# Optimization experiments

Measured on AMD Instinct MI355X. Metric: run time of the kernel, lower is better.

## Reference

```python
import jax, jax.numpy as jnp
import numpy as np

H = 8        # heads
DH = 64      # dim_head
EPS = 1e-5   # LayerNorm eps (torch default)


def setup_inputs() -> dict:
    key = jax.random.key(0)
    k0, k1, k2, k3, k4 = jax.random.split(key, 5)
    b, l, n, dim = 2, 8, 256, 512
    inner = H * DH
    return {
        "xyzs": jax.random.normal(k0, (b, l, n, 3), dtype=jnp.float32),
        "features": jax.random.normal(k1, (b, l, n, dim), dtype=jnp.float32),
        "ln_gamma": jnp.ones((dim,), dtype=jnp.float32),
        "ln_beta": jnp.zeros((dim,), dtype=jnp.float32),
        "w_qkv": jax.random.normal(k2, (dim, 3 * inner), dtype=jnp.float32) * 0.02,
        "w_sp": jax.random.normal(k3, (3, DH), dtype=jnp.float32) * 0.3,
        "w_out": jax.random.normal(k4, (inner, dim), dtype=jnp.float32) * 0.02,
        "b_out": jnp.zeros((dim,), dtype=jnp.float32),
    }


def reference(xyzs, features, ln_gamma, ln_beta, w_qkv, w_sp, w_out, b_out):
    b, l, n, dim = features.shape
    m = l * n
    inner = H * DH
    scale = DH ** (-0.5)

    # LayerNorm over last dim (biased variance, eps=1e-5)
    mu = jnp.mean(features, axis=-1, keepdims=True)
    var = jnp.var(features, axis=-1, keepdims=True)
    normed = (features - mu) * jax.lax.rsqrt(var + EPS) * ln_gamma + ln_beta

    # qkv projection, chunk into q,k,v, reshape 'b l n (h d) -> b h (l n) d'
    qkv = normed.reshape(b, m, dim) @ w_qkv            # [b, m, 3*inner]
    def split_heads(t):
        return t.reshape(b, m, H, DH).transpose(0, 2, 1, 3)  # [b, h, m, d]
    q = split_heads(qkv[..., :inner])
    k = split_heads(qkv[..., inner:2 * inner])
    v = split_heads(qkv[..., 2 * inner:])

    dots = jnp.einsum('bhid,bhjd->bhij', q, k) * scale  # [b, h, m, m]
    attn = jax.nn.softmax(dots, axis=-1)
    v_out = jnp.einsum('bhij,bhjd->bhid', attn, v)      # [b, h, m, d]

    # pairwise coordinate deltas: delta[b,i,j,c] = xyz[b,j,c] - xyz[b,i,c]
    xyz_f = xyzs.reshape(b, m, 3)
    delta = xyz_f[:, None, :, :] - xyz_f[:, :, None, :]  # [b, m, m, 3]
    # attention-weighted aggregation over j (avoids [b,h,m,m,3] intermediate)
    agg = jnp.einsum('bhij,bijc->bhic', attn, delta)     # [b, h, m, 3]
    disp = agg @ w_sp                                    # [b, h, m, DH]

    out = v_out + disp                                   # [b, h, m, DH]
    out = out.transpose(0, 2, 1, 3).reshape(b, m, inner) # 'b h m d -> b m (h d)'
    out = jax.nn.gelu(out @ w_out + b_out, approximate=False)
    return out.reshape(b, l, n, dim) + features
```

## Files before the change

### kernel.cpp

```cpp
#include <hip/hip_runtime.h>
#include <hip/hip_bf16.h>
#include <math.h>

#define BB   2
#define MM   2048
#define DIM  512
#define NH   8
#define DHd  64
#define NQK  1536
#define ROWS 4096
#define NROW 32768
#define SPLITK 3

typedef __hip_bfloat16 bf16;
typedef __attribute__((ext_vector_type(8))) short bf16x8;
typedef __attribute__((ext_vector_type(4))) float f32x4;
typedef __attribute__((ext_vector_type(16))) float f32x16;
typedef __attribute__((ext_vector_type(8))) unsigned short us8;
typedef __attribute__((ext_vector_type(4))) unsigned int u32x4;

__device__ __forceinline__ unsigned short f2bf_bits(float x) {
    bf16 h = __float2bfloat16(x);
    return *(unsigned short*)&h;
}
__device__ __forceinline__ float bf2f(unsigned short u) {
    unsigned int v = ((unsigned int)u) << 16;
    return __uint_as_float(v);
}
__device__ __forceinline__ unsigned cvtpk_bf16(float lo, float hi) {
    unsigned r;
    asm("v_cvt_pk_bf16_f32 %0, %1, %2" : "=v"(r) : "v"(lo), "v"(hi));
    return r;
}
__device__ __forceinline__ void pl32swap(unsigned &a, unsigned &b) {
    asm volatile("v_permlane32_swap_b32 %0, %1" : "+v"(a), "+v"(b));
}

__global__ __launch_bounds__(256) void pre_kernel(
    const float* __restrict__ feat, const float* __restrict__ gamma,
    const float* __restrict__ beta, unsigned short* __restrict__ normed,
    const float* __restrict__ wqkv, const float* __restrict__ wout,
    unsigned short* __restrict__ wqkvT, unsigned short* __restrict__ woutT)
{
    __shared__ float st[64][65];
    int b = blockIdx.x;
    int tid = threadIdx.x;
    if (b < ROWS / 4) {
        int w = tid >> 6, lane = tid & 63;
        int row = b * 4 + w;
        const float* fr = feat + (size_t)row * DIM + lane * 8;
        float4 v0 = *(const float4*)fr;
        float4 v1 = *(const float4*)(fr + 4);
        float s  = v0.x + v0.y + v0.z + v0.w + v1.x + v1.y + v1.z + v1.w;
        float ss = v0.x*v0.x + v0.y*v0.y + v0.z*v0.z + v0.w*v0.w
                 + v1.x*v1.x + v1.y*v1.y + v1.z*v1.z + v1.w*v1.w;
        #pragma unroll
        for (int o = 32; o >= 1; o >>= 1) { s += __shfl_xor(s, o); ss += __shfl_xor(ss, o); }
        float mu  = s * (1.0f / DIM);
        float var = ss * (1.0f / DIM) - mu * mu;
        float inv = rsqrtf(var + 1e-5f);
        const float* gp = gamma + lane * 8;
        const float* bp = beta  + lane * 8;
        float4 g0 = *(const float4*)gp, g1 = *(const float4*)(gp + 4);
        float4 e0 = *(const float4*)bp, e1 = *(const float4*)(bp + 4);
        unsigned short ov[8];
        ov[0] = f2bf_bits((v0.x - mu) * inv * g0.x + e0.x);
        ov[1] = f2bf_bits((v0.y - mu) * inv * g0.y + e0.y);
        ov[2] = f2bf_bits((v0.z - mu) * inv * g0.z + e0.z);
        ov[3] = f2bf_bits((v0.w - mu) * inv * g0.w + e0.w);
        ov[4] = f2bf_bits((v1.x - mu) * inv * g1.x + e1.x);
        ov[5] = f2bf_bits((v1.y - mu) * inv * g1.y + e1.y);
        ov[6] = f2bf_bits((v1.z - mu) * inv * g1.z + e1.z);
        ov[7] = f2bf_bits((v1.w - mu) * inv * g1.w + e1.w);
        *(us8*)&normed[(size_t)row * DIM + lane * 8] = *(us8*)ov;
        return;
    }
    int idx = b - ROWS / 4;
    const float* in; unsigned short* out; int N, n0;
    if (idx < 192) { in = wqkv; out = wqkvT; N = NQK; n0 = (idx >> 3) * 64; }
    else { idx -= 192; in = wout; out = woutT; N = DIM; n0 = (idx >> 3) * 64; }
    int k0 = (idx & 7) * 64;
    #pragma unroll
    for (int p = 0; p < 16; p++) {
        int e = tid + p * 256;
        int r = e >> 6, c = e & 63;
        st[r][c] = in[(size_t)(k0 + r) * N + n0 + c];
    }
    __syncthreads();
    #pragma unroll
    for (int p = 0; p < 16; p++) {
        int e = tid + p * 256;
        int nr = e >> 6, kc = e & 63;
        out[(size_t)(n0 + nr) * DIM + k0 + kc] = f2bf_bits(st[kc][nr]);
    }
}

__global__ __launch_bounds__(256) void qkv_gemm(
    const unsigned short* __restrict__ A, const unsigned short* __restrict__ BT,
    unsigned short* __restrict__ qd, unsigned short* __restrict__ kd,
    unsigned short* __restrict__ vd)
{
    __shared__ __align__(16) unsigned short sA[128 * 72];
    __shared__ __align__(16) unsigned short sB[64 * 72];
    int tid = threadIdx.x;
    int r0 = blockIdx.x * 128;
    int n0 = blockIdx.y * 64;
    int chunk = n0 >> 9;
    int h     = (n0 & 511) >> 6;
    int w = tid >> 6, lane = tid & 63;
    int wm = w >> 1, wn = w & 1;
    int ln15 = lane & 15, quad = lane >> 4;

    int arow = tid >> 1, acol = (tid & 1) * 32;
    int brow = tid >> 2, bcol = (tid & 3) * 16;

    f32x4 acc[4][2] = {};
    us8 ra[4], rb[2];

    #pragma unroll
    for (int u = 0; u < 4; u++)
        ra[u] = *(const us8*)&A[(size_t)(r0 + arow) * DIM + acol + u * 8];
    #pragma unroll
    for (int u = 0; u < 2; u++)
        rb[u] = *(const us8*)&BT[(size_t)(n0 + brow) * DIM + bcol + u * 8];

    for (int k0 = 0; k0 < DIM; k0 += 64) {
        __syncthreads();
        #pragma unroll
        for (int u = 0; u < 4; u++) *(us8*)&sA[arow * 72 + acol + u * 8] = ra[u];
        #pragma unroll
        for (int u = 0; u < 2; u++) *(us8*)&sB[brow * 72 + bcol + u * 8] = rb[u];
        __syncthreads();
        int kn = k0 + 64;
        if (kn < DIM) {
            #pragma unroll
            for (int u = 0; u < 4; u++)
                ra[u] = *(const us8*)&A[(size_t)(r0 + arow) * DIM + kn + acol + u * 8];
            #pragma unroll
            for (int u = 0; u < 2; u++)
                rb[u] = *(const us8*)&BT[(size_t)(n0 + brow) * DIM + kn + bcol + u * 8];
        }
        bf16x8 fa[4][2], fb[2][2];
        #pragma unroll
        for (int i = 0; i < 4; i++)
            #pragma unroll
            for (int kk = 0; kk < 2; kk++)
                fa[i][kk] = *(const bf16x8*)&sA[(wm * 64 + i * 16 + ln15) * 72 + kk * 32 + quad * 8];
        #pragma unroll
        for (int j = 0; j < 2; j++)
            #pragma unroll
            for (int kk = 0; kk < 2; kk++)
                fb[j][kk] = *(const bf16x8*)&sB[(wn * 32 + j * 16 + ln15) * 72 + kk * 32 + quad * 8];
        if (chunk == 2) {
            #pragma unroll
            for (int kk = 0; kk < 2; kk++)
                #pragma unroll
                for (int i = 0; i < 4; i++)
                    #pragma unroll
                    for (int j = 0; j < 2; j++)
                        acc[i][j] = __builtin_amdgcn_mfma_f32_16x16x32_bf16(fa[i][kk], fb[j][kk], acc[i][j], 0, 0, 0);
        } else {
            #pragma unroll
            for (int kk = 0; kk < 2; kk++)
                #pragma unroll
                for (int i = 0; i < 4; i++)
                    #pragma unroll
                    for (int j = 0; j < 2; j++)
                        acc[i][j] = __builtin_amdgcn_mfma_f32_16x16x32_bf16(fb[j][kk], fa[i][kk], acc[i][j], 0, 0, 0);
        }
    }

    if (chunk == 2) {
        #pragma unroll
        for (int i = 0; i < 4; i++) {
            int gm = r0 + wm * 64 + i * 16 + quad * 4;
            int bb = gm >> 11, mm = gm & 2047;
            #pragma unroll
            for (int j = 0; j < 2; j++) {
                int d = wn * 32 + j * 16 + ln15;
                ushort4 pk;
                pk.x = f2bf_bits(acc[i][j][0]);
                pk.y = f2bf_bits(acc[i][j][1]);
                pk.z = f2bf_bits(acc[i][j][2]);
                pk.w = f2bf_bits(acc[i][j][3]);
                *(ushort4*)&vd[((size_t)(bb * NH + h) * DHd + d) * MM + mm] = pk;
            }
        }
    } else {
        unsigned short* dst = (chunk == 0) ? qd : kd;
        float sc = (chunk == 0) ? 0.125f : 1.0f;
        #pragma unroll
        for (int i = 0; i < 4; i++) {
            int gm = r0 + wm * 64 + i * 16 + ln15;
            int bb = gm >> 11, mm = gm & 2047;
            #pragma unroll
            for (int j = 0; j < 2; j++) {
                int d0 = wn * 32 + j * 16 + quad * 4;
                ushort4 pk;
                pk.x = f2bf_bits(acc[i][j][0] * sc);
                pk.y = f2bf_bits(acc[i][j][1] * sc);
                pk.z = f2bf_bits(acc[i][j][2] * sc);
                pk.w = f2bf_bits(acc[i][j][3] * sc);
                *(ushort4*)&dst[((size_t)(bb * NH + h) * MM + mm) * DHd + d0] = pk;
            }
        }
    }
}

__global__ __launch_bounds__(256, 3) void attn_kernel(
    const unsigned short* __restrict__ qg, const unsigned short* __restrict__ kg,
    const unsigned short* __restrict__ vg, const float* __restrict__ xyzs,
    unsigned short* __restrict__ obuf, float* __restrict__ lbuf)
{
    __shared__ __align__(16) unsigned short sK[64 * 72];
    __shared__ __align__(16) unsigned short sVT[96 * 72];

    int tid = threadIdx.x;
    int bh = blockIdx.y; int bb = bh >> 3;
    int i0 = blockIdx.x * 128;
    int ks = blockIdx.z;
    int w = tid >> 6;
    int lane = tid & 63;
    int ln31 = lane & 31;
    int hi   = lane >> 5;
    int hi8  = hi * 8;

    for (int e = tid; e < 28 * 72; e += 256) sVT[68 * 72 + e] = 0;
    if (tid < 64) sVT[67 * 72 + tid] = 0x3F80;

    bf16x8 aq[4];
    {
        const unsigned short* q0 = qg + ((size_t)bh * MM + i0 + w * 32 + ln31) * DHd + hi8;
        #pragma unroll
        for (int kc = 0; kc < 4; kc++)
            aq[kc] = *(const bf16x8*)(q0 + kc * 16);
    }

    f32x16 ot[3] = {};

    const unsigned short* kbase = kg + (size_t)bh * MM * DHd;
    const unsigned short* vbase = vg + (size_t)bh * DHd * MM;
    int jbeg = ks * 704;
    int jend = (ks == 2) ? MM : jbeg + 704;

    int srow = tid >> 2, scol16 = (tid & 3) * 16;

    us8 rk0, rk1, rv0, rv1;
    float rx = 0.f;
    {
        const unsigned short* src = kbase + (size_t)jbeg * DHd;
        rk0 = *(const us8*)&src[(size_t)tid * 16];
        rk1 = *(const us8*)&src[(size_t)tid * 16 + 8];
        const unsigned short* vs = vbase + jbeg;
        rv0 = *(const us8*)&vs[(size_t)srow * MM + scol16];
        rv1 = *(const us8*)&vs[(size_t)srow * MM + scol16 + 8];
        if (tid < 192) rx = xyzs[((size_t)bb * MM + jbeg) * 3 + tid];
    }

    for (int jt = jbeg; jt < jend; jt += 64) {
        __syncthreads();
        *(us8*)&sK[srow * 72 + scol16]      = rk0;
        *(us8*)&sK[srow * 72 + scol16 + 8]  = rk1;
        *(us8*)&sVT[srow * 72 + scol16]     = rv0;
        *(us8*)&sVT[srow * 72 + scol16 + 8] = rv1;
        if (tid < 192) {
            int key = tid / 3, c = tid - key * 3;
            sVT[(64 + c) * 72 + key] = f2bf_bits(rx);
        }
        __syncthreads();
        int jn = jt + 64;
        if (jn < jend) {
            const unsigned short* src = kbase + (size_t)jn * DHd;
            rk0 = *(const us8*)&src[(size_t)tid * 16];
            rk1 = *(const us8*)&src[(size_t)tid * 16 + 8];
            const unsigned short* vs = vbase + jn;
            rv0 = *(const us8*)&vs[(size_t)srow * MM + scol16];
            rv1 = *(const us8*)&vs[(size_t)srow * MM + scol16 + 8];
            if (tid < 192) rx = xyzs[((size_t)bb * MM + jn) * 3 + tid];
        }

        #pragma unroll
        for (int b = 0; b < 2; b++) {
            f32x16 zz = {};
            #pragma unroll
            for (int kc = 0; kc < 4; kc++) {
                bf16x8 kf = *(const bf16x8*)&sK[(b * 32 + ln31) * 72 + kc * 16 + hi8];
                zz = __builtin_amdgcn_mfma_f32_32x32x16_bf16(kf, aq[kc], zz, 0, 0, 0);
            }
            unsigned c_[8];
            #pragma unroll
            for (int j = 0; j < 8; j++)
                c_[j] = cvtpk_bf16(__expf(zz[2 * j]), __expf(zz[2 * j + 1]));
            unsigned x0 = c_[0], x2 = c_[2]; pl32swap(x0, x2);
            unsigned x1 = c_[1], x3 = c_[3]; pl32swap(x1, x3);
            unsigned y0 = c_[4], y2 = c_[6]; pl32swap(y0, y2);
            unsigned y1 = c_[5], y3 = c_[7]; pl32swap(y1, y3);
            u32x4 xv = {x0, x1, x2, x3};
            u32x4 yv = {y0, y1, y2, y3};
            bf16x8 X = *(bf16x8*)&xv;
            bf16x8 Y = *(bf16x8*)&yv;
            #pragma unroll
            for (int vb = 0; vb < 3; vb++) {
                bf16x8 v0 = *(const bf16x8*)&sVT[(vb * 32 + ln31) * 72 + b * 32 + hi8];
                bf16x8 v1 = *(const bf16x8*)&sVT[(vb * 32 + ln31) * 72 + b * 32 + 16 + hi8];
                ot[vb] = __builtin_amdgcn_mfma_f32_32x32x16_bf16(v0, X, ot[vb], 0, 0, 0);
                ot[vb] = __builtin_amdgcn_mfma_f32_32x32x16_bf16(v1, Y, ot[vb], 0, 0, 0);
            }
        }
    }

    size_t kso = (size_t)ks * NROW;
    size_t row = (size_t)bh * MM + i0 + w * 32 + ln31;
    unsigned short* orow = obuf + (kso + row) * 72;
    #pragma unroll
    for (int vb = 0; vb < 2; vb++) {
        #pragma unroll
        for (int rq = 0; rq < 4; rq++) {
            ushort4 pk;
            pk.x = f2bf_bits(ot[vb][rq * 4 + 0]);
            pk.y = f2bf_bits(ot[vb][rq * 4 + 1]);
            pk.z = f2bf_bits(ot[vb][rq * 4 + 2]);
            pk.w = f2bf_bits(ot[vb][rq * 4 + 3]);
            *(ushort4*)&orow[vb * 32 + rq * 8 + hi * 4] = pk;
        }
    }
    if (hi == 0) {
        orow[64] = f2bf_bits(ot[2][0]);
        orow[65] = f2bf_bits(ot[2][1]);
        orow[66] = f2bf_bits(ot[2][2]);
        lbuf[kso + row] = ot[2][3];
    }
}

__global__ __launch_bounds__(256) void merge_kernel(
    const unsigned short* __restrict__ obuf, const float* __restrict__ lbuf,
    const float* __restrict__ xyzs, const float* __restrict__ wsp,
    unsigned short* __restrict__ attn_out)
{
    __shared__ float sW[3][64];
    int tid = threadIdx.x;
    if (tid < 192) sW[tid >> 6][tid & 63] = wsp[tid];
    __syncthreads();
    int r   = blockIdx.x * 64 + (tid >> 2);
    int d0  = (tid & 3) * 16;
    int bh = r >> 11, qrow = r & 2047, bb = bh >> 3, hh = bh & 7;
    const unsigned short* p0 = obuf + (size_t)r * 72;
    const unsigned short* p1 = p0 + (size_t)NROW * 72;
    const unsigned short* p2 = p1 + (size_t)NROW * 72;
    float invl = 1.f / (lbuf[r] + lbuf[NROW + r] + lbuf[2 * NROW + r]);
    size_t xb = ((size_t)bb * MM + qrow) * 3;
    float gx = (bf2f(p0[64]) + bf2f(p1[64]) + bf2f(p2[64])) * invl - xyzs[xb + 0];
    float gy = (bf2f(p0[65]) + bf2f(p1[65]) + bf2f(p2[65])) * invl - xyzs[xb + 1];
    float gz = (bf2f(p0[66]) + bf2f(p1[66]) + bf2f(p2[66])) * invl - xyzs[xb + 2];
    us8 a0 = *(const us8*)&p0[d0];
    us8 a1 = *(const us8*)&p0[d0 + 8];
    us8 b0 = *(const us8*)&p1[d0];
    us8 b1 = *(const us8*)&p1[d0 + 8];
    us8 c0 = *(const us8*)&p2[d0];
    us8 c1 = *(const us8*)&p2[d0 + 8];
    unsigned short outv[16];
    #pragma unroll
    for (int e = 0; e < 8; e++) {
        int d = d0 + e;
        float v = (bf2f(a0[e]) + bf2f(b0[e]) + bf2f(c0[e])) * invl
                + gx * sW[0][d] + gy * sW[1][d] + gz * sW[2][d];
        outv[e] = f2bf_bits(v);
    }
    #pragma unroll
    for (int e = 0; e < 8; e++) {
        int d = d0 + 8 + e;
        float v = (bf2f(a1[e]) + bf2f(b1[e]) + bf2f(c1[e])) * invl
                + gx * sW[0][d] + gy * sW[1][d] + gz * sW[2][d];
        outv[8 + e] = f2bf_bits(v);
    }
    unsigned short* dst = attn_out + ((size_t)bb * MM + qrow) * DIM + hh * DHd + d0;
    *(us8*)dst       = *(us8*)&outv[0];
    *(us8*)(dst + 8) = *(us8*)&outv[8];
}

__global__ __launch_bounds__(256) void out_gemm(
    const unsigned short* __restrict__ A, const unsigned short* __restrict__ BT,
    const float* __restrict__ bias, const float* __restrict__ feat,
    float* __restrict__ out)
{
    __shared__ __align__(16) unsigned short sA[64 * 72];
    __shared__ __align__(16) unsigned short sB[64 * 72];
    int tid = threadIdx.x;
    int r0 = blockIdx.x * 64, n0 = blockIdx.y * 64;
    int w = tid >> 6, lane = tid & 63;
    int wm = w >> 1, wn = w & 1;
    int ln15 = lane & 15, quad = lane >> 4;

    int srow = tid >> 2, scol = (tid & 3) * 16;

    f32x4 acc[2][2] = {};
    us8 ra[2], rb[2];

    #pragma unroll
    for (int u = 0; u < 2; u++) {
        ra[u] = *(const us8*)&A[(size_t)(r0 + srow) * DIM + scol + u * 8];
        rb[u] = *(const us8*)&BT[(size_t)(n0 + srow) * DIM + scol + u * 8];
    }

    for (int k0 = 0; k0 < DIM; k0 += 64) {
        __syncthreads();
        #pragma unroll
        for (int u = 0; u < 2; u++) {
            *(us8*)&sA[srow * 72 + scol + u * 8] = ra[u];
            *(us8*)&sB[srow * 72 + scol + u * 8] = rb[u];
        }
        __syncthreads();
        int kn = k0 + 64;
        if (kn < DIM) {
            #pragma unroll
            for (int u = 0; u < 2; u++) {
                ra[u] = *(const us8*)&A[(size_t)(r0 + srow) * DIM + kn + scol + u * 8];
                rb[u] = *(const us8*)&BT[(size_t)(n0 + srow) * DIM + kn + scol + u * 8];
            }
        }
        bf16x8 af[2][2], bf_[2][2];
        #pragma unroll
        for (int i = 0; i < 2; i++)
            #pragma unroll
            for (int kk = 0; kk < 2; kk++)
                af[i][kk] = *(const bf16x8*)&sA[(wm * 32 + i * 16 + ln15) * 72 + kk * 32 + quad * 8];
        #pragma unroll
        for (int j = 0; j < 2; j++)
            #pragma unroll
            for (int kk = 0; kk < 2; kk++)
                bf_[j][kk] = *(const bf16x8*)&sB[(wn * 32 + j * 16 + ln15) * 72 + kk * 32 + quad * 8];
        #pragma unroll
        for (int kk = 0; kk < 2; kk++)
            #pragma unroll
            for (int i = 0; i < 2; i++)
                #pragma unroll
                for (int j = 0; j < 2; j++)
                    acc[i][j] = __builtin_amdgcn_mfma_f32_16x16x32_bf16(af[i][kk], bf_[j][kk], acc[i][j], 0, 0, 0);
    }

    #pragma unroll
    for (int i = 0; i < 2; i++) {
        #pragma unroll
        for (int reg = 0; reg < 4; reg++) {
            int gr = r0 + wm * 32 + i * 16 + quad * 4 + reg;
            #pragma unroll
            for (int j = 0; j < 2; j++) {
                int c = n0 + wn * 32 + j * 16 + ln15;
                float x = acc[i][j][reg] + bias[c];
                float g = 0.5f * x * (1.f + erff(x * 0.70710678118f));
                out[(size_t)gr * DIM + c] = g + feat[(size_t)gr * DIM + c];
            }
        }
    }
}

extern "C" void kernel_launch(void* const* d_in, const int* in_sizes, int n_in,
                              void* d_out, int out_size, void* d_ws, size_t ws_size,
                              hipStream_t stream)
{
    const float* xyzs  = (const float*)d_in[0];
    const float* feat  = (const float*)d_in[1];
    const float* gamma = (const float*)d_in[2];
    const float* beta  = (const float*)d_in[3];
    const float* wqkv  = (const float*)d_in[4];
    const float* wsp   = (const float*)d_in[5];
    const float* wout  = (const float*)d_in[6];
    const float* bout  = (const float*)d_in[7];
    float* out = (float*)d_out;

    unsigned short* ws16 = (unsigned short*)d_ws;
    const size_t SEGS = (size_t)ROWS * DIM;
    unsigned short* normed = ws16;
    unsigned short* qb     = ws16 + SEGS;
    unsigned short* kb     = ws16 + 2 * SEGS;
    unsigned short* vb     = ws16 + 3 * SEGS;
    unsigned short* wqkvT  = ws16 + 4 * SEGS;
    unsigned short* woutT  = wqkvT + (size_t)NQK * DIM;
    unsigned short* obuf   = woutT + (size_t)DIM * DIM;
    float*          lbuf   = (float*)(obuf + (size_t)SPLITK * NROW * 72);

    pre_kernel<<<ROWS / 4 + 256, 256, 0, stream>>>(feat, gamma, beta, normed,
                                                   wqkv, wout, wqkvT, woutT);
    qkv_gemm<<<dim3(32, 24), 256, 0, stream>>>(normed, wqkvT, qb, kb, vb);
    attn_kernel<<<dim3(16, 16, SPLITK), 256, 0, stream>>>(qb, kb, vb, xyzs, obuf, lbuf);
    merge_kernel<<<512, 256, 0, stream>>>(obuf, lbuf, xyzs, wsp, normed);
    out_gemm<<<dim3(64, 8), 256, 0, stream>>>(normed, woutT, bout, feat, out);
}
```

Measured before the change: 141.8 us.

## Drop split-K attention and fuse merge epilogue into attention kernel

```diff
diff --git a/kernel.cpp b/kernel.cpp
--- a/kernel.cpp
+++ b/kernel.cpp
@@ -9,8 +9,6 @@
 #define DHd  64
 #define NQK  1536
 #define ROWS 4096
-#define NROW 32768
-#define SPLITK 3
 
 typedef __hip_bfloat16 bf16;
 typedef __attribute__((ext_vector_type(8))) short bf16x8;
@@ -207,26 +205,27 @@
     }
 }
 
-__global__ __launch_bounds__(256, 3) void attn_kernel(
+__global__ __launch_bounds__(128, 1) void attn_kernel(
     const unsigned short* __restrict__ qg, const unsigned short* __restrict__ kg,
     const unsigned short* __restrict__ vg, const float* __restrict__ xyzs,
-    unsigned short* __restrict__ obuf, float* __restrict__ lbuf)
+    const float* __restrict__ wsp, unsigned short* __restrict__ attn_out)
 {
     __shared__ __align__(16) unsigned short sK[64 * 72];
     __shared__ __align__(16) unsigned short sVT[96 * 72];
+    __shared__ float sW[3][64];
 
     int tid = threadIdx.x;
-    int bh = blockIdx.y; int bb = bh >> 3;
-    int i0 = blockIdx.x * 128;
-    int ks = blockIdx.z;
+    int bh = blockIdx.y; int bb = bh >> 3; int hh = bh & 7;
+    int i0 = blockIdx.x * 64;
     int w = tid >> 6;
     int lane = tid & 63;
     int ln31 = lane & 31;
     int hi   = lane >> 5;
     int hi8  = hi * 8;
 
-    for (int e = tid; e < 28 * 72; e += 256) sVT[68 * 72 + e] = 0;
+    for (int e = tid; e < 28 * 72; e += 128) sVT[68 * 72 + e] = 0;
     if (tid < 64) sVT[67 * 72 + tid] = 0x3F80;
+    for (int e = tid; e < 192; e += 128) sW[e >> 6][e & 63] = wsp[e];
 
     bf16x8 aq[4];
     {
@@ -240,43 +239,47 @@
 
     const unsigned short* kbase = kg + (size_t)bh * MM * DHd;
     const unsigned short* vbase = vg + (size_t)bh * DHd * MM;
-    int jbeg = ks * 704;
-    int jend = (ks == 2) ? MM : jbeg + 704;
-
-    int srow = tid >> 2, scol16 = (tid & 3) * 16;
-
-    us8 rk0, rk1, rv0, rv1;
-    float rx = 0.f;
+
+    int srow = tid >> 1, scolB = (tid & 1) * 32;
+    int key0 = tid / 3, c0 = tid - key0 * 3;
+    int e1 = tid + 128;
+    int key1 = e1 / 3, c1 = e1 - key1 * 3;
+
+    us8 rk[4], rv[4];
+    float rx0 = 0.f, rx1 = 0.f;
     {
-        const unsigned short* src = kbase + (size_t)jbeg * DHd;
-        rk0 = *(const us8*)&src[(size_t)tid * 16];
-        rk1 = *(const us8*)&src[(size_t)tid * 16 + 8];
-        const unsigned short* vs = vbase + jbeg;
-        rv0 = *(const us8*)&vs[(size_t)srow * MM + scol16];
-        rv1 = *(const us8*)&vs[(size_t)srow * MM + scol16 + 8];
-        if (tid < 192) rx = xyzs[((size_t)bb * MM + jbeg) * 3 + tid];
-    }
-
-    for (int jt = jbeg; jt < jend; jt += 64) {
-        __syncthreads();
-        *(us8*)&sK[srow * 72 + scol16]      = rk0;
-        *(us8*)&sK[srow * 72 + scol16 + 8]  = rk1;
-        *(us8*)&sVT[srow * 72 + scol16]     = rv0;
-        *(us8*)&sVT[srow * 72 + scol16 + 8] = rv1;
-        if (tid < 192) {
-            int key = tid / 3, c = tid - key * 3;
-            sVT[(64 + c) * 72 + key] = f2bf_bits(rx);
-        }
+        const unsigned short* ks = kbase + (size_t)srow * DHd + scolB;
+        const unsigned short* vs = vbase + (size_t)srow * MM + scolB;
+        #pragma unroll
+        for (int u = 0; u < 4; u++) {
+            rk[u] = *(const us8*)(ks + u * 8);
+            rv[u] = *(const us8*)(vs + u * 8);
+        }
+        rx0 = xyzs[(size_t)bb * MM * 3 + tid];
+        if (tid < 64) rx1 = xyzs[(size_t)bb * MM * 3 + e1];
+    }
+
+    for (int jt = 0; jt < MM; jt += 64) {
+        __syncthreads();
+        #pragma unroll
+        for (int u = 0; u < 4; u++) {
+            *(us8*)&sK[srow * 72 + scolB + u * 8]  = rk[u];
+            *(us8*)&sVT[srow * 72 + scolB + u * 8] = rv[u];
+        }
+        sVT[(64 + c0) * 72 + key0] = f2bf_bits(rx0);
+        if (tid < 64) sVT[(64 + c1) * 72 + key1] = f2bf_bits(rx1);
         __syncthreads();
         int jn = jt + 64;
-        if (jn < jend) {
-            const unsigned short* src = kbase + (size_t)jn * DHd;
-            rk0 = *(const us8*)&src[(size_t)tid * 16];
-            rk1 = *(const us8*)&src[(size_t)tid * 16 + 8];
-            const unsigned short* vs = vbase + jn;
-            rv0 = *(const us8*)&vs[(size_t)srow * MM + scol16];
-            rv1 = *(const us8*)&vs[(size_t)srow * MM + scol16 + 8];
-            if (tid < 192) rx = xyzs[((size_t)bb * MM + jn) * 3 + tid];
+        if (jn < MM) {
+            const unsigned short* ks = kbase + (size_t)(jn + srow) * DHd + scolB;
+            const unsigned short* vs = vbase + (size_t)srow * MM + jn + scolB;
+            #pragma unroll
+            for (int u = 0; u < 4; u++) {
+                rk[u] = *(const us8*)(ks + u * 8);
+                rv[u] = *(const us8*)(vs + u * 8);
+            }
+            rx0 = xyzs[((size_t)bb * MM + jn) * 3 + tid];
+            if (tid < 64) rx1 = xyzs[((size_t)bb * MM + jn) * 3 + e1];
         }
 
         #pragma unroll
@@ -309,73 +312,29 @@
         }
     }
 
-    size_t kso = (size_t)ks * NROW;
-    size_t row = (size_t)bh * MM + i0 + w * 32 + ln31;
-    unsigned short* orow = obuf + (kso + row) * 72;
+    int gq = i0 + w * 32 + ln31;
+    float invl = 1.f / __shfl(ot[2][3], ln31);
+    size_t xb = ((size_t)bb * MM + gq) * 3;
+    float gx = __shfl(ot[2][0], ln31) * invl - xyzs[xb + 0];
+    float gy = __shfl(ot[2][1], ln31) * invl - xyzs[xb + 1];
+    float gz = __shfl(ot[2][2], ln31) * invl - xyzs[xb + 2];
+    unsigned short* dst = attn_out + ((size_t)bb * MM + gq) * DIM + hh * DHd;
     #pragma unroll
     for (int vb = 0; vb < 2; vb++) {
         #pragma unroll
         for (int rq = 0; rq < 4; rq++) {
+            int d0 = vb * 32 + rq * 8 + hi * 4;
             ushort4 pk;
-            pk.x = f2bf_bits(ot[vb][rq * 4 + 0]);
-            pk.y = f2bf_bits(ot[vb][rq * 4 + 1]);
-            pk.z = f2bf_bits(ot[vb][rq * 4 + 2]);
-            pk.w = f2bf_bits(ot[vb][rq * 4 + 3]);
-            *(ushort4*)&orow[vb * 32 + rq * 8 + hi * 4] = pk;
-        }
-    }
-    if (hi == 0) {
-        orow[64] = f2bf_bits(ot[2][0]);
-        orow[65] = f2bf_bits(ot[2][1]);
-        orow[66] = f2bf_bits(ot[2][2]);
-        lbuf[kso + row] = ot[2][3];
-    }
-}
-
-__global__ __launch_bounds__(256) void merge_kernel(
-    const unsigned short* __restrict__ obuf, const float* __restrict__ lbuf,
-    const float* __restrict__ xyzs, const float* __restrict__ wsp,
-    unsigned short* __restrict__ attn_out)
-{
-    __shared__ float sW[3][64];
-    int tid = threadIdx.x;
-    if (tid < 192) sW[tid >> 6][tid & 63] = wsp[tid];
-    __syncthreads();
-    int r   = blockIdx.x * 64 + (tid >> 2);
-    int d0  = (tid & 3) * 16;
-    int bh = r >> 11, qrow = r & 2047, bb = bh >> 3, hh = bh & 7;
-    const unsigned short* p0 = obuf + (size_t)r * 72;
-    const unsigned short* p1 = p0 + (size_t)NROW * 72;
-    const unsigned short* p2 = p1 + (size_t)NROW * 72;
-    float invl = 1.f / (lbuf[r] + lbuf[NROW + r] + lbuf[2 * NROW + r]);
-    size_t xb = ((size_t)bb * MM + qrow) * 3;
-    float gx = (bf2f(p0[64]) + bf2f(p1[64]) + bf2f(p2[64])) * invl - xyzs[xb + 0];
-    float gy = (bf2f(p0[65]) + bf2f(p1[65]) + bf2f(p2[65])) * invl - xyzs[xb + 1];
-    float gz = (bf2f(p0[66]) + bf2f(p1[66]) + bf2f(p2[66])) * invl - xyzs[xb + 2];
-    us8 a0 = *(const us8*)&p0[d0];
-    us8 a1 = *(const us8*)&p0[d0 + 8];
-    us8 b0 = *(const us8*)&p1[d0];
-    us8 b1 = *(const us8*)&p1[d0 + 8];
-    us8 c0 = *(const us8*)&p2[d0];
-    us8 c1 = *(const us8*)&p2[d0 + 8];
-    unsigned short outv[16];
-    #pragma unroll
-    for (int e = 0; e < 8; e++) {
-        int d = d0 + e;
-        float v = (bf2f(a0[e]) + bf2f(b0[e]) + bf2f(c0[e])) * invl
-                + gx * sW[0][d] + gy * sW[1][d] + gz * sW[2][d];
-        outv[e] = f2bf_bits(v);
-    }
-    #pragma unroll
-    for (int e = 0; e < 8; e++) {
-        int d = d0 + 8 + e;
-        float v = (bf2f(a1[e]) + bf2f(b1[e]) + bf2f(c1[e])) * invl
-                + gx * sW[0][d] + gy * sW[1][d] + gz * sW[2][d];
-        outv[8 + e] = f2bf_bits(v);
-    }
-    unsigned short* dst = attn_out + ((size_t)bb * MM + qrow) * DIM + hh * DHd + d0;
-    *(us8*)dst       = *(us8*)&outv[0];
-    *(us8*)(dst + 8) = *(us8*)&outv[8];
+            #pragma unroll
+            for (int j = 0; j < 4; j++) {
+                int d = d0 + j;
+                float v = ot[vb][rq * 4 + j] * invl
+                        + gx * sW[0][d] + gy * sW[1][d] + gz * sW[2][d];
+                ((unsigned short*)&pk)[j] = f2bf_bits(v);
+            }
+            *(ushort4*)&dst[d0] = pk;
+        }
+    }
 }
 
 __global__ __launch_bounds__(256) void out_gemm(
@@ -476,13 +435,10 @@
     unsigned short* vb     = ws16 + 3 * SEGS;
     unsigned short* wqkvT  = ws16 + 4 * SEGS;
     unsigned short* woutT  = wqkvT + (size_t)NQK * DIM;
-    unsigned short* obuf   = woutT + (size_t)DIM * DIM;
-    float*          lbuf   = (float*)(obuf + (size_t)SPLITK * NROW * 72);
 
     pre_kernel<<<ROWS / 4 + 256, 256, 0, stream>>>(feat, gamma, beta, normed,
                                                    wqkv, wout, wqkvT, woutT);
     qkv_gemm<<<dim3(32, 24), 256, 0, stream>>>(normed, wqkvT, qb, kb, vb);
-    attn_kernel<<<dim3(16, 16, SPLITK), 256, 0, stream>>>(qb, kb, vb, xyzs, obuf, lbuf);
-    merge_kernel<<<512, 256, 0, stream>>>(obuf, lbuf, xyzs, wsp, normed);
+    attn_kernel<<<dim3(32, 16), 128, 0, stream>>>(qb, kb, vb, xyzs, wsp, normed);
     out_gemm<<<dim3(64, 8), 256, 0, stream>>>(normed, woutT, bout, feat, out);
 }
```

Result: slower. 154.6 us (+9.0%).

## Split attention keys four ways, fold log2e into Q scale, use exp2

Applied to the files above, without the earlier changes.

```diff
diff --git a/kernel.cpp b/kernel.cpp
--- a/kernel.cpp
+++ b/kernel.cpp
@@ -10,7 +10,7 @@
 #define NQK  1536
 #define ROWS 4096
 #define NROW 32768
-#define SPLITK 3
+#define SPLITK 4
 
 typedef __hip_bfloat16 bf16;
 typedef __attribute__((ext_vector_type(8))) short bf16x8;
@@ -188,7 +188,7 @@
         }
     } else {
         unsigned short* dst = (chunk == 0) ? qd : kd;
-        float sc = (chunk == 0) ? 0.125f : 1.0f;
+        float sc = (chunk == 0) ? 0.18033688f : 1.0f;
         #pragma unroll
         for (int i = 0; i < 4; i++) {
             int gm = r0 + wm * 64 + i * 16 + ln15;
@@ -207,7 +207,7 @@
     }
 }
 
-__global__ __launch_bounds__(256, 3) void attn_kernel(
+__global__ __launch_bounds__(256, 4) void attn_kernel(
     const unsigned short* __restrict__ qg, const unsigned short* __restrict__ kg,
     const unsigned short* __restrict__ vg, const float* __restrict__ xyzs,
     unsigned short* __restrict__ obuf, float* __restrict__ lbuf)
@@ -219,7 +219,7 @@
     int bh = blockIdx.y; int bb = bh >> 3;
     int i0 = blockIdx.x * 128;
     int ks = blockIdx.z;
-    int w = tid >> 6;
+    int wid = tid >> 6;
     int lane = tid & 63;
     int ln31 = lane & 31;
     int hi   = lane >> 5;
@@ -230,7 +230,7 @@
 
     bf16x8 aq[4];
     {
-        const unsigned short* q0 = qg + ((size_t)bh * MM + i0 + w * 32 + ln31) * DHd + hi8;
+        const unsigned short* q0 = qg + ((size_t)bh * MM + i0 + wid * 32 + ln31) * DHd + hi8;
         #pragma unroll
         for (int kc = 0; kc < 4; kc++)
             aq[kc] = *(const bf16x8*)(q0 + kc * 16);
@@ -240,42 +240,40 @@
 
     const unsigned short* kbase = kg + (size_t)bh * MM * DHd;
     const unsigned short* vbase = vg + (size_t)bh * DHd * MM;
-    int jbeg = ks * 704;
-    int jend = (ks == 2) ? MM : jbeg + 704;
-
-    int srow = tid >> 2, scol16 = (tid & 3) * 16;
+    int jbeg = ks * (MM / SPLITK);
+
+    int srow = tid >> 2, scolB = (tid & 3) * 16;
+    int key0 = tid / 3, c0 = tid - key0 * 3;
 
     us8 rk0, rk1, rv0, rv1;
     float rx = 0.f;
     {
-        const unsigned short* src = kbase + (size_t)jbeg * DHd;
-        rk0 = *(const us8*)&src[(size_t)tid * 16];
-        rk1 = *(const us8*)&src[(size_t)tid * 16 + 8];
-        const unsigned short* vs = vbase + jbeg;
-        rv0 = *(const us8*)&vs[(size_t)srow * MM + scol16];
-        rv1 = *(const us8*)&vs[(size_t)srow * MM + scol16 + 8];
+        const unsigned short* ksrc = kbase + (size_t)(jbeg + srow) * DHd + scolB;
+        const unsigned short* vsrc = vbase + (size_t)srow * MM + jbeg + scolB;
+        rk0 = *(const us8*)ksrc;
+        rk1 = *(const us8*)(ksrc + 8);
+        rv0 = *(const us8*)vsrc;
+        rv1 = *(const us8*)(vsrc + 8);
         if (tid < 192) rx = xyzs[((size_t)bb * MM + jbeg) * 3 + tid];
     }
 
-    for (int jt = jbeg; jt < jend; jt += 64) {
-        __syncthreads();
-        *(us8*)&sK[srow * 72 + scol16]      = rk0;
-        *(us8*)&sK[srow * 72 + scol16 + 8]  = rk1;
-        *(us8*)&sVT[srow * 72 + scol16]     = rv0;
-        *(us8*)&sVT[srow * 72 + scol16 + 8] = rv1;
-        if (tid < 192) {
-            int key = tid / 3, c = tid - key * 3;
-            sVT[(64 + c) * 72 + key] = f2bf_bits(rx);
-        }
+    for (int t = 0; t < MM / SPLITK / 64; ++t) {
+        int jt = jbeg + t * 64;
+        __syncthreads();
+        *(us8*)&sK[srow * 72 + scolB]      = rk0;
+        *(us8*)&sK[srow * 72 + scolB + 8]  = rk1;
+        *(us8*)&sVT[srow * 72 + scolB]     = rv0;
+        *(us8*)&sVT[srow * 72 + scolB + 8] = rv1;
+        if (tid < 192) sVT[(64 + c0) * 72 + key0] = f2bf_bits(rx);
         __syncthreads();
         int jn = jt + 64;
-        if (jn < jend) {
-            const unsigned short* src = kbase + (size_t)jn * DHd;
-            rk0 = *(const us8*)&src[(size_t)tid * 16];
-            rk1 = *(const us8*)&src[(size_t)tid * 16 + 8];
-            const unsigned short* vs = vbase + jn;
-            rv0 = *(const us8*)&vs[(size_t)srow * MM + scol16];
-            rv1 = *(const us8*)&vs[(size_t)srow * MM + scol16 + 8];
+        if (jn < jbeg + MM / SPLITK) {
+            const unsigned short* ksrc = kbase + (size_t)(jn + srow) * DHd + scolB;
+            const unsigned short* vsrc = vbase + (size_t)srow * MM + jn + scolB;
+            rk0 = *(const us8*)ksrc;
+            rk1 = *(const us8*)(ksrc + 8);
+            rv0 = *(const us8*)vsrc;
+            rv1 = *(const us8*)(vsrc + 8);
             if (tid < 192) rx = xyzs[((size_t)bb * MM + jn) * 3 + tid];
         }
 
@@ -290,7 +288,7 @@
             unsigned c_[8];
             #pragma unroll
             for (int j = 0; j < 8; j++)
-                c_[j] = cvtpk_bf16(__expf(zz[2 * j]), __expf(zz[2 * j + 1]));
+                c_[j] = cvtpk_bf16(exp2f(zz[2 * j]), exp2f(zz[2 * j + 1]));
             unsigned x0 = c_[0], x2 = c_[2]; pl32swap(x0, x2);
             unsigned x1 = c_[1], x3 = c_[3]; pl32swap(x1, x3);
             unsigned y0 = c_[4], y2 = c_[6]; pl32swap(y0, y2);
@@ -310,7 +308,7 @@
     }
 
     size_t kso = (size_t)ks * NROW;
-    size_t row = (size_t)bh * MM + i0 + w * 32 + ln31;
+    size_t row = (size_t)bh * MM + i0 + wid * 32 + ln31;
     unsigned short* orow = obuf + (kso + row) * 72;
     #pragma unroll
     for (int vb = 0; vb < 2; vb++) {
@@ -347,29 +345,32 @@
     const unsigned short* p0 = obuf + (size_t)r * 72;
     const unsigned short* p1 = p0 + (size_t)NROW * 72;
     const unsigned short* p2 = p1 + (size_t)NROW * 72;
-    float invl = 1.f / (lbuf[r] + lbuf[NROW + r] + lbuf[2 * NROW + r]);
+    const unsigned short* p3 = p2 + (size_t)NROW * 72;
+    float invl = 1.f / (lbuf[r] + lbuf[NROW + r] + lbuf[2 * NROW + r] + lbuf[3 * NROW + r]);
     size_t xb = ((size_t)bb * MM + qrow) * 3;
-    float gx = (bf2f(p0[64]) + bf2f(p1[64]) + bf2f(p2[64])) * invl - xyzs[xb + 0];
-    float gy = (bf2f(p0[65]) + bf2f(p1[65]) + bf2f(p2[65])) * invl - xyzs[xb + 1];
-    float gz = (bf2f(p0[66]) + bf2f(p1[66]) + bf2f(p2[66])) * invl - xyzs[xb + 2];
+    float gx = (bf2f(p0[64]) + bf2f(p1[64]) + bf2f(p2[64]) + bf2f(p3[64])) * invl - xyzs[xb + 0];
+    float gy = (bf2f(p0[65]) + bf2f(p1[65]) + bf2f(p2[65]) + bf2f(p3[65])) * invl - xyzs[xb + 1];
+    float gz = (bf2f(p0[66]) + bf2f(p1[66]) + bf2f(p2[66]) + bf2f(p3[66])) * invl - xyzs[xb + 2];
     us8 a0 = *(const us8*)&p0[d0];
     us8 a1 = *(const us8*)&p0[d0 + 8];
     us8 b0 = *(const us8*)&p1[d0];
     us8 b1 = *(const us8*)&p1[d0 + 8];
     us8 c0 = *(const us8*)&p2[d0];
     us8 c1 = *(const us8*)&p2[d0 + 8];
+    us8 e0 = *(const us8*)&p3[d0];
+    us8 e1 = *(const us8*)&p3[d0 + 8];
     unsigned short outv[16];
     #pragma unroll
     for (int e = 0; e < 8; e++) {
         int d = d0 + e;
-        float v = (bf2f(a0[e]) + bf2f(b0[e]) + bf2f(c0[e])) * invl
+        float v = (bf2f(a0[e]) + bf2f(b0[e]) + bf2f(c0[e]) + bf2f(e0[e])) * invl
                 + gx * sW[0][d] + gy * sW[1][d] + gz * sW[2][d];
         outv[e] = f2bf_bits(v);
     }
     #pragma unroll
     for (int e = 0; e < 8; e++) {
         int d = d0 + 8 + e;
-        float v = (bf2f(a1[e]) + bf2f(b1[e]) + bf2f(c1[e])) * invl
+        float v = (bf2f(a1[e]) + bf2f(b1[e]) + bf2f(c1[e]) + bf2f(e1[e])) * invl
                 + gx * sW[0][d] + gy * sW[1][d] + gz * sW[2][d];
         outv[8 + e] = f2bf_bits(v);
     }
```

New measurement: 143.1 us. Within noise of the previous version (+0.9%).
